# Kernel tuning notes

Measured on AMD Instinct MI355X. Metric: run time of the kernel, lower is better.

The kernel has to match this reference:

```python
import jax, jax.numpy as jnp
import numpy as np


def conv2d(x, w, stride=1, padding=0):
    # x: [N,Ci,H,W], w: [Co,Ci,Kh,Kw]
    return jax.lax.conv_general_dilated(
        x, w, window_strides=(stride, stride),
        padding=[(padding, padding), (padding, padding)],
        dimension_numbers=('NCHW', 'OIHW', 'NCHW'))


def adder2d(x, w, stride=1, padding=0):
    """AdderNet L1-distance conv: out[n,co,ho,wo] = -sum_{ci,kh,kw} |x_patch - w[co,ci,kh,kw]|."""
    N, Ci, H, W = x.shape
    Co, _, K, _ = w.shape
    xp = jnp.pad(x, ((0, 0), (0, 0), (padding, padding), (padding, padding)))
    Ho = (H + 2 * padding - K) // stride + 1
    Wo = (W + 2 * padding - K) // stride + 1
    acc = jnp.zeros((N, Co, Ho, Wo), x.dtype)
    for kh in range(K):  # small fixed loop over kernel taps (<=9)
        for kw in range(K):
            xs = xp[:, :, kh:kh + Ho * stride:stride, kw:kw + Wo * stride:stride]  # [N,Ci,Ho,Wo]
            diff = jnp.abs(xs[:, None] - w[None, :, :, kh, kw, None, None])  # [N,Co,Ci,Ho,Wo]
            acc = acc - diff.sum(axis=2)
    return acc


def batchnorm(x, gamma, beta, mean, var, eps=1e-5):
    inv = gamma / jnp.sqrt(var + eps)
    return x * inv[None, :, None, None] + (beta - mean * inv)[None, :, None, None]


def setup_inputs() -> dict:
    key = jax.random.key(0)
    ks = jax.random.split(key, 16)
    N, C, H, W = 4, 128, 28, 28
    inp = {
        'x': jax.random.normal(ks[0], (N, C, H, W), jnp.float32),
        'w_shift1': jax.random.normal(ks[1], (C, C, 1, 1), jnp.float32) * 0.1,
        'w_add1': jax.random.normal(ks[2], (C, C, 1, 1), jnp.float32) * 0.1,
        'bn1_gamma': jax.random.uniform(ks[3], (C,), jnp.float32, 0.5, 1.5),
        'bn1_beta': jax.random.normal(ks[4], (C,), jnp.float32) * 0.1,
        'bn1_mean': jax.random.normal(ks[5], (C,), jnp.float32),
        'bn1_var': jax.random.uniform(ks[6], (C,), jnp.float32, 0.5, 1.5),
        'w_shift2': jax.random.normal(ks[7], (C, C, 3, 3), jnp.float32) * 0.05,
        'w_add2': jax.random.normal(ks[8], (C, C, 3, 3), jnp.float32) * 0.05,
        'bn2_gamma': jax.random.uniform(ks[9], (C,), jnp.float32, 0.5, 1.5),
        'bn2_beta': jax.random.normal(ks[10], (C,), jnp.float32) * 0.1,
        'bn2_mean': jax.random.normal(ks[11], (C,), jnp.float32),
        'bn2_var': jax.random.uniform(ks[12], (C,), jnp.float32, 0.5, 1.5),
    }
    return inp


def reference(x, w_shift1, w_add1, bn1_gamma, bn1_beta, bn1_mean, bn1_var,
              w_shift2, w_add2, bn2_gamma, bn2_beta, bn2_mean, bn2_var):
    identity = x
    # conv1: 1x1 shift conv -> 1x1 adder
    out = conv2d(x, w_shift1, stride=1, padding=0)
    out = adder2d(out, w_add1, stride=1, padding=0)
    out = jax.nn.relu(batchnorm(out, bn1_gamma, bn1_beta, bn1_mean, bn1_var))
    # conv2: 3x3 shift conv (stride=1, pad=1) -> 3x3 adder (stride=1, pad=1)
    out = conv2d(out, w_shift2, stride=1, padding=1)
    out = adder2d(out, w_add2, stride=1, padding=1)
    out = jax.nn.relu(batchnorm(out, bn2_gamma, bn2_beta, bn2_mean, bn2_var))
    return jax.nn.relu(out + identity)
```

## Files before the change

kernel.cpp:

```cpp
#include <hip/hip_runtime.h>
#include <math.h>

constexpr int C   = 128;
constexpr int HW  = 784;
constexpr int PW  = 32;
constexpr int PH  = 30;
constexpr int PHW = PW * PH;

#define ABS_ACC(acc, d) asm("v_add_f32 %0, %0, abs(%1)" : "+v"(acc) : "v"(d))

__device__ inline void tile_map2(int wg, int& n, int& h0, int& w0) {
    int region = wg & 7;
    int idx    = wg >> 3;
    n = region >> 1;
    int half = region & 1;
    int th = half * 7 + idx / 14;
    int tw = idx % 14;
    h0 = th * 2;
    w0 = tw * 2;
}

__device__ inline void tile_map44(int wg, int& n, int& h0, int& w0, int& co0) {
    int region = wg & 7;
    int idx    = wg >> 3;
    n   = region >> 1;
    co0 = (region & 1) * 64;
    int th = idx / 7, tw = idx % 7;
    h0 = th * 4;
    w0 = tw * 4;
}

__device__ inline void zero_border2(float* plane, int h0, int w0) {
    if (h0 == 0) {
        plane[w0 + 1] = 0.f; plane[w0 + 2] = 0.f;
        if (w0 == 0)  plane[0]  = 0.f;
        if (w0 == 26) plane[29] = 0.f;
    }
    if (h0 == 26) {
        plane[29 * PW + w0 + 1] = 0.f; plane[29 * PW + w0 + 2] = 0.f;
        if (w0 == 0)  plane[29 * PW]      = 0.f;
        if (w0 == 26) plane[29 * PW + 29] = 0.f;
    }
    if (w0 == 0)  { plane[(h0 + 1) * PW]      = 0.f; plane[(h0 + 2) * PW]      = 0.f; }
    if (w0 == 26) { plane[(h0 + 1) * PW + 29] = 0.f; plane[(h0 + 2) * PW + 29] = 0.f; }
}

__device__ inline void zero_border44(float* plane, int h0, int w0) {
    if (h0 == 0) {
#pragma unroll
        for (int c = 0; c < 4; ++c) plane[w0 + 1 + c] = 0.f;
        if (w0 == 0)  plane[0]  = 0.f;
        if (w0 == 24) plane[29] = 0.f;
    }
    if (h0 == 24) {
#pragma unroll
        for (int c = 0; c < 4; ++c) plane[29 * PW + w0 + 1 + c] = 0.f;
        if (w0 == 0)  plane[29 * PW]      = 0.f;
        if (w0 == 24) plane[29 * PW + 29] = 0.f;
    }
    if (w0 == 0) {
#pragma unroll
        for (int r = 0; r < 4; ++r) plane[(h0 + 1 + r) * PW] = 0.f;
    }
    if (w0 == 24) {
#pragma unroll
        for (int r = 0; r < 4; ++r) plane[(h0 + 1 + r) * PW + 29] = 0.f;
    }
}

__global__ __launch_bounds__(256) void reorder_w(const float* __restrict__ w2,
                                                 const float* __restrict__ a2,
                                                 const float* __restrict__ w1,
                                                 const float* __restrict__ a1,
                                                 float* __restrict__ w2r,
                                                 float* __restrict__ a2r,
                                                 float* __restrict__ w1r,
                                                 float* __restrict__ a1r) {
    int idx = blockIdx.x * 256 + threadIdx.x;
    const int T9 = C * C * 9;
    const int T1 = C * C;
    if (idx < 2 * T9) {
        const float* src = w2; float* dst = w2r;
        if (idx >= T9) { idx -= T9; src = a2; dst = a2r; }
        int co = idx & 127;
        int r  = idx >> 7;
        int k  = r % 9;
        int ci = r / 9;
        dst[idx] = src[(co * C + ci) * 9 + k];
        return;
    }
    idx -= 2 * T9;
    if (idx >= 2 * T1) return;
    const float* src = w1; float* dst = w1r;
    if (idx >= T1) { idx -= T1; src = a1; dst = a1r; }
    int co = idx & 127;
    int ci = idx >> 7;
    dst[idx] = src[co * C + ci];
}

__global__ __launch_bounds__(256, 8) void stage1(const float* __restrict__ x,
                                                 const float* __restrict__ w1r,
                                                 const float* __restrict__ a1r,
                                                 const float* __restrict__ g1,
                                                 const float* __restrict__ b1,
                                                 const float* __restrict__ m1,
                                                 const float* __restrict__ v1,
                                                 float* __restrict__ t1p) {
    __shared__ float Xs[C][4];
    __shared__ float Ys[C][4];
    __shared__ float Rs[C][4];
    int n, h0, w0;
    tile_map2(blockIdx.x, n, h0, w0);
    int t   = threadIdx.x;
    int co  = t & 127;
    int ciq = t >> 7;
    int ci0 = ciq * 64;

#pragma unroll
    for (int e = t; e < 512; e += 256) {
        int ci = e >> 2, p = e & 3, r = p >> 1, c = p & 1;
        Xs[ci][p] = x[(n * C + ci) * HW + (h0 + r) * 28 + w0 + c];
    }
    __syncthreads();

    float4 a = make_float4(0.f, 0.f, 0.f, 0.f);
    const float* wp = w1r + co;
#pragma unroll 4
    for (int i = 0; i < 64; ++i) {
        int ci = ci0 + i;
        float wv = wp[ci * C];
        float4 xv = *reinterpret_cast<const float4*>(&Xs[ci][0]);
        a.x = fmaf(xv.x, wv, a.x);
        a.y = fmaf(xv.y, wv, a.y);
        a.z = fmaf(xv.z, wv, a.z);
        a.w = fmaf(xv.w, wv, a.w);
    }
    if (ciq) *reinterpret_cast<float4*>(&Rs[co][0]) = a;
    __syncthreads();
    if (ciq == 0) {
        float4 r = *reinterpret_cast<const float4*>(&Rs[co][0]);
        a.x += r.x; a.y += r.y; a.z += r.z; a.w += r.w;
        *reinterpret_cast<float4*>(&Ys[co][0]) = a;
    }
    __syncthreads();

    float d0 = 0.f, d1 = 0.f, d2 = 0.f, d3 = 0.f;
    const float* ap = a1r + co;
#pragma unroll 4
    for (int i = 0; i < 64; ++i) {
        int ci = ci0 + i;
        float av = ap[ci * C];
        float4 yv = *reinterpret_cast<const float4*>(&Ys[ci][0]);
        float e0 = yv.x - av; ABS_ACC(d0, e0);
        float e1 = yv.y - av; ABS_ACC(d1, e1);
        float e2 = yv.z - av; ABS_ACC(d2, e2);
        float e3 = yv.w - av; ABS_ACC(d3, e3);
    }
    if (ciq) *reinterpret_cast<float4*>(&Rs[co][0]) = make_float4(d0, d1, d2, d3);
    __syncthreads();
    if (ciq == 0) {
        float4 r = *reinterpret_cast<const float4*>(&Rs[co][0]);
        d0 += r.x; d1 += r.y; d2 += r.z; d3 += r.w;
        float inv = g1[co] / sqrtf(v1[co] + 1e-5f);
        float off = b1[co] - m1[co] * inv;
        float* plane = t1p + (n * C + co) * PHW;
        float* dst = plane + (h0 + 1) * PW + (w0 + 1);
        dst[0]      = fmaxf(-d0 * inv + off, 0.f);
        dst[1]      = fmaxf(-d1 * inv + off, 0.f);
        dst[PW + 0] = fmaxf(-d2 * inv + off, 0.f);
        dst[PW + 1] = fmaxf(-d3 * inv + off, 0.f);
        zero_border2(plane, h0, w0);
    }
}

__global__ __launch_bounds__(512, 8) void conv3x3(const float* __restrict__ t1p,
                                                  const float* __restrict__ w2r,
                                                  float* __restrict__ t2p) {
    __shared__ float Rs[7][64][16];
    int n, h0, w0, co0;
    tile_map44(blockIdx.x, n, h0, w0, co0);
    int t   = threadIdx.x;
    int col = t & 63;
    int co  = co0 + col;
    int ciq = t >> 6;
    int ci0u = __builtin_amdgcn_readfirstlane(ciq * 16);

    const float* sp0 = t1p + n * C * PHW + h0 * PW + w0;
    const float* wb  = w2r + co;
    float acc[16];
#pragma unroll
    for (int j = 0; j < 16; ++j) acc[j] = 0.f;

#pragma unroll 2
    for (int i = 0; i < 16; ++i) {
        int ci = ci0u + i;
        const float* wp = wb + ci * 9 * C;
        float wk[9];
#pragma unroll
        for (int k = 0; k < 9; ++k) wk[k] = wp[k * C];
        const float* sp = sp0 + ci * PHW;
        float xr[6][6];
#pragma unroll
        for (int r = 0; r < 6; ++r)
#pragma unroll
            for (int c = 0; c < 6; ++c) xr[r][c] = sp[r * PW + c];
#pragma unroll
        for (int kh = 0; kh < 3; ++kh)
#pragma unroll
            for (int kw = 0; kw < 3; ++kw) {
                float wv = wk[kh * 3 + kw];
#pragma unroll
                for (int pr = 0; pr < 4; ++pr)
#pragma unroll
                    for (int pc = 0; pc < 4; ++pc)
                        acc[pr * 4 + pc] = fmaf(xr[pr + kh][pc + kw], wv, acc[pr * 4 + pc]);
            }
    }
    if (ciq) {
#pragma unroll
        for (int j = 0; j < 4; ++j)
            *reinterpret_cast<float4*>(&Rs[ciq - 1][col][j * 4]) =
                make_float4(acc[j * 4], acc[j * 4 + 1], acc[j * 4 + 2], acc[j * 4 + 3]);
    }
    __syncthreads();
    if (ciq == 0) {
#pragma unroll
        for (int q = 0; q < 7; ++q)
#pragma unroll
            for (int j = 0; j < 16; ++j) acc[j] += Rs[q][col][j];
        float* plane = t2p + (n * C + co) * PHW;
        float* dst = plane + (h0 + 1) * PW + (w0 + 1);
#pragma unroll
        for (int pr = 0; pr < 4; ++pr)
#pragma unroll
            for (int pc = 0; pc < 4; ++pc) dst[pr * PW + pc] = acc[pr * 4 + pc];
        zero_border44(plane, h0, w0);
    }
}

__global__ __launch_bounds__(512, 8) void adder3x3(const float* __restrict__ t2p,
                                                   const float* __restrict__ a2r,
                                                   const float* __restrict__ x0,
                                                   const float* __restrict__ g2,
                                                   const float* __restrict__ b2,
                                                   const float* __restrict__ m2,
                                                   const float* __restrict__ v2,
                                                   float* __restrict__ out) {
    __shared__ float Rs[7][64][16];
    int n, h0, w0, co0;
    tile_map44(blockIdx.x, n, h0, w0, co0);
    int t   = threadIdx.x;
    int col = t & 63;
    int co  = co0 + col;
    int ciq = t >> 6;
    int ci0u = __builtin_amdgcn_readfirstlane(ciq * 16);

    const float* sp0 = t2p + n * C * PHW + h0 * PW + w0;
    const float* ab  = a2r + co;
    float acc[16];
#pragma unroll
    for (int j = 0; j < 16; ++j) acc[j] = 0.f;

#pragma unroll 2
    for (int i = 0; i < 16; ++i) {
        int ci = ci0u + i;
        const float* wp = ab + ci * 9 * C;
        float wk[9];
#pragma unroll
        for (int k = 0; k < 9; ++k) wk[k] = wp[k * C];
        const float* sp = sp0 + ci * PHW;
        float xr[6][6];
#pragma unroll
        for (int r = 0; r < 6; ++r)
#pragma unroll
            for (int c = 0; c < 6; ++c) xr[r][c] = sp[r * PW + c];
#pragma unroll
        for (int kh = 0; kh < 3; ++kh)
#pragma unroll
            for (int kw = 0; kw < 3; ++kw) {
                float wv = wk[kh * 3 + kw];
#pragma unroll
                for (int pr = 0; pr < 4; ++pr)
#pragma unroll
                    for (int pc = 0; pc < 4; ++pc) {
                        float e = xr[pr + kh][pc + kw] - wv;
                        ABS_ACC(acc[pr * 4 + pc], e);
                    }
            }
    }
    if (ciq) {
#pragma unroll
        for (int j = 0; j < 4; ++j)
            *reinterpret_cast<float4*>(&Rs[ciq - 1][col][j * 4]) =
                make_float4(acc[j * 4], acc[j * 4 + 1], acc[j * 4 + 2], acc[j * 4 + 3]);
    }
    __syncthreads();
    if (ciq == 0) {
#pragma unroll
        for (int q = 0; q < 7; ++q)
#pragma unroll
            for (int j = 0; j < 16; ++j) acc[j] += Rs[q][col][j];
        float inv = g2[co] / sqrtf(v2[co] + 1e-5f);
        float off = b2[co] - m2[co] * inv;
        int base = (n * C + co) * HW + h0 * 28 + w0;
#pragma unroll
        for (int pr = 0; pr < 4; ++pr)
#pragma unroll
            for (int pc = 0; pc < 4; ++pc) {
                float z = fmaxf(-acc[pr * 4 + pc] * inv + off, 0.f);
                z += x0[base + pr * 28 + pc];
                out[base + pr * 28 + pc] = fmaxf(z, 0.f);
            }
    }
}

extern "C" void kernel_launch(void* const* d_in, const int* in_sizes, int n_in,
                              void* d_out, int out_size, void* d_ws, size_t ws_size,
                              hipStream_t stream) {
    const float* x   = (const float*)d_in[0];
    const float* w1  = (const float*)d_in[1];
    const float* a1  = (const float*)d_in[2];
    const float* g1  = (const float*)d_in[3];
    const float* b1  = (const float*)d_in[4];
    const float* m1  = (const float*)d_in[5];
    const float* v1  = (const float*)d_in[6];
    const float* w2  = (const float*)d_in[7];
    const float* a2  = (const float*)d_in[8];
    const float* g2  = (const float*)d_in[9];
    const float* b2  = (const float*)d_in[10];
    const float* m2  = (const float*)d_in[11];
    const float* v2  = (const float*)d_in[12];
    float* out = (float*)d_out;

    float* ws  = (float*)d_ws;
    float* t1p = ws;
    float* t2p = t1p + 4 * C * PHW;
    float* w2r = t2p + 4 * C * PHW;
    float* a2r = w2r + C * C * 9;
    float* w1r = a2r + C * C * 9;
    float* a1r = w1r + C * C;

    const int reorder_total = 2 * C * C * 9 + 2 * C * C;
    reorder_w<<<(reorder_total + 255) / 256, 256, 0, stream>>>(w2, a2, w1, a1, w2r, a2r, w1r, a1r);
    stage1<<<784, 256, 0, stream>>>(x, w1r, a1r, g1, b1, m1, v1, t1p);
    conv3x3<<<392, 512, 0, stream>>>(t1p, w2r, t2p);
    adder3x3<<<392, 512, 0, stream>>>(t2p, a2r, x, g2, b2, m2, v2, out);
}
```

Baseline: 73.16 us.

## Stage 3x3 input tile in LDS and split output channels into quarters

```diff
diff --git a/kernel.cpp b/kernel.cpp
--- a/kernel.cpp
+++ b/kernel.cpp
@@ -20,11 +20,13 @@
     w0 = tw * 2;
 }
 
-__device__ inline void tile_map44(int wg, int& n, int& h0, int& w0, int& co0) {
-    int region = wg & 7;
-    int idx    = wg >> 3;
-    n   = region >> 1;
-    co0 = (region & 1) * 64;
+__device__ inline void tile_map16(int wg, int& n, int& h0, int& w0, int& co0) {
+    int r3   = wg & 7;
+    int unit = wg >> 3;
+    n = r3 >> 1;
+    int coq = ((r3 & 1) << 1) | (unit & 1);
+    co0 = coq * 32;
+    int idx = unit >> 1;
     int th = idx / 7, tw = idx % 7;
     h0 = th * 4;
     w0 = tw * 4;
@@ -173,37 +175,47 @@
     }
 }
 
-__global__ __launch_bounds__(512, 8) void conv3x3(const float* __restrict__ t1p,
+__global__ __launch_bounds__(256, 4) void conv3x3(const float* __restrict__ t1p,
                                                   const float* __restrict__ w2r,
                                                   float* __restrict__ t2p) {
-    __shared__ float Rs[7][64][16];
+    __shared__ float Xl[C][6][8];
+    __shared__ float Rs[7][32][16];
     int n, h0, w0, co0;
-    tile_map44(blockIdx.x, n, h0, w0, co0);
+    tile_map16(blockIdx.x, n, h0, w0, co0);
     int t   = threadIdx.x;
-    int col = t & 63;
+    int col = t & 31;
     int co  = co0 + col;
-    int ciq = t >> 6;
-    int ci0u = __builtin_amdgcn_readfirstlane(ciq * 16);
+    int ciq = t >> 5;
+    int ci0 = ciq * 16;
 
     const float* sp0 = t1p + n * C * PHW + h0 * PW + w0;
-    const float* wb  = w2r + co;
+    for (int e = t; e < 1536; e += 256) {
+        int ci = e / 12, rem = e - ci * 12, r = rem >> 1, hf = rem & 1;
+        *reinterpret_cast<float4*>(&Xl[ci][r][hf * 4]) =
+            *reinterpret_cast<const float4*>(sp0 + ci * PHW + r * PW + hf * 4);
+    }
+    __syncthreads();
+
+    const float* wb = w2r + co;
     float acc[16];
 #pragma unroll
     for (int j = 0; j < 16; ++j) acc[j] = 0.f;
 
 #pragma unroll 2
     for (int i = 0; i < 16; ++i) {
-        int ci = ci0u + i;
+        int ci = ci0 + i;
         const float* wp = wb + ci * 9 * C;
         float wk[9];
 #pragma unroll
         for (int k = 0; k < 9; ++k) wk[k] = wp[k * C];
-        const float* sp = sp0 + ci * PHW;
         float xr[6][6];
 #pragma unroll
-        for (int r = 0; r < 6; ++r)
-#pragma unroll
-            for (int c = 0; c < 6; ++c) xr[r][c] = sp[r * PW + c];
+        for (int r = 0; r < 6; ++r) {
+            float4 q = *reinterpret_cast<const float4*>(&Xl[ci][r][0]);
+            float2 s = *reinterpret_cast<const float2*>(&Xl[ci][r][4]);
+            xr[r][0] = q.x; xr[r][1] = q.y; xr[r][2] = q.z;
+            xr[r][3] = q.w; xr[r][4] = s.x; xr[r][5] = s.y;
+        }
 #pragma unroll
         for (int kh = 0; kh < 3; ++kh)
 #pragma unroll
@@ -216,6 +228,7 @@
                         acc[pr * 4 + pc] = fmaf(xr[pr + kh][pc + kw], wv, acc[pr * 4 + pc]);
             }
     }
+
     if (ciq) {
 #pragma unroll
         for (int j = 0; j < 4; ++j)
@@ -238,7 +251,7 @@
     }
 }
 
-__global__ __launch_bounds__(512, 8) void adder3x3(const float* __restrict__ t2p,
+__global__ __launch_bounds__(256, 4) void adder3x3(const float* __restrict__ t2p,
                                                    const float* __restrict__ a2r,
                                                    const float* __restrict__ x0,
                                                    const float* __restrict__ g2,
@@ -246,34 +259,44 @@
                                                    const float* __restrict__ m2,
                                                    const float* __restrict__ v2,
                                                    float* __restrict__ out) {
-    __shared__ float Rs[7][64][16];
+    __shared__ float Xl[C][6][8];
+    __shared__ float Rs[7][32][16];
     int n, h0, w0, co0;
-    tile_map44(blockIdx.x, n, h0, w0, co0);
+    tile_map16(blockIdx.x, n, h0, w0, co0);
     int t   = threadIdx.x;
-    int col = t & 63;
+    int col = t & 31;
     int co  = co0 + col;
-    int ciq = t >> 6;
-    int ci0u = __builtin_amdgcn_readfirstlane(ciq * 16);
+    int ciq = t >> 5;
+    int ci0 = ciq * 16;
 
     const float* sp0 = t2p + n * C * PHW + h0 * PW + w0;
-    const float* ab  = a2r + co;
+    for (int e = t; e < 1536; e += 256) {
+        int ci = e / 12, rem = e - ci * 12, r = rem >> 1, hf = rem & 1;
+        *reinterpret_cast<float4*>(&Xl[ci][r][hf * 4]) =
+            *reinterpret_cast<const float4*>(sp0 + ci * PHW + r * PW + hf * 4);
+    }
+    __syncthreads();
+
+    const float* ab = a2r + co;
     float acc[16];
 #pragma unroll
     for (int j = 0; j < 16; ++j) acc[j] = 0.f;
 
 #pragma unroll 2
     for (int i = 0; i < 16; ++i) {
-        int ci = ci0u + i;
+        int ci = ci0 + i;
         const float* wp = ab + ci * 9 * C;
         float wk[9];
 #pragma unroll
         for (int k = 0; k < 9; ++k) wk[k] = wp[k * C];
-        const float* sp = sp0 + ci * PHW;
         float xr[6][6];
 #pragma unroll
-        for (int r = 0; r < 6; ++r)
-#pragma unroll
-            for (int c = 0; c < 6; ++c) xr[r][c] = sp[r * PW + c];
+        for (int r = 0; r < 6; ++r) {
+            float4 q = *reinterpret_cast<const float4*>(&Xl[ci][r][0]);
+            float2 s = *reinterpret_cast<const float2*>(&Xl[ci][r][4]);
+            xr[r][0] = q.x; xr[r][1] = q.y; xr[r][2] = q.z;
+            xr[r][3] = q.w; xr[r][4] = s.x; xr[r][5] = s.y;
+        }
 #pragma unroll
         for (int kh = 0; kh < 3; ++kh)
 #pragma unroll
@@ -288,6 +311,7 @@
                     }
             }
     }
+
     if (ciq) {
 #pragma unroll
         for (int j = 0; j < 4; ++j)
@@ -343,6 +367,6 @@
     const int reorder_total = 2 * C * C * 9 + 2 * C * C;
     reorder_w<<<(reorder_total + 255) / 256, 256, 0, stream>>>(w2, a2, w1, a1, w2r, a2r, w1r, a1r);
     stage1<<<784, 256, 0, stream>>>(x, w1r, a1r, g1, b1, m1, v1, t1p);
-    conv3x3<<<392, 512, 0, stream>>>(t1p, w2r, t2p);
-    adder3x3<<<392, 512, 0, stream>>>(t2p, a2r, x, g2, b2, m2, v2, out);
-}
+    conv3x3<<<784, 256, 0, stream>>>(t1p, w2r, t2p);
+    adder3x3<<<784, 256, 0, stream>>>(t2p, a2r, x, g2, b2, m2, v2, out);
+}
```

Result: faster. 69.84 us (-4.5%).
